# Kernel tuning notes

Measured on AMD Instinct MI355X. Metric: run time of the kernel, lower is better.

Reference implementation:

```python
import jax, jax.numpy as jnp
import numpy as np

N_NODES = 100000
N_EDGES = 1600000
IN_DIM = 128
OUT_DIM = 128
ALPHA = 0.2  # leaky relu negative slope
EPS = 9e-15


def setup_inputs() -> dict:
    key = jax.random.key(0)
    k1, k2, k3, k4, k5 = jax.random.split(key, 5)
    x = jax.random.normal(k1, (N_NODES, IN_DIM), dtype=jnp.float32)
    src = jax.random.randint(k2, (N_EDGES,), 0, N_NODES)
    dst = jax.random.randint(k3, (N_EDGES,), 0, N_NODES)
    edge_index = jnp.stack([src, dst]).astype(jnp.int64)
    # xavier-normal-ish params
    W = jax.random.normal(k4, (IN_DIM, OUT_DIM), dtype=jnp.float32) * (1.414 * np.sqrt(2.0 / (IN_DIM + OUT_DIM)))
    attn = jax.random.normal(k5, (1, 2 * OUT_DIM), dtype=jnp.float32) * (1.414 * np.sqrt(2.0 / (1 + 2 * OUT_DIM)))
    return {"x": x, "edge_index": edge_index, "W": W, "attn": attn}


def reference(x, edge_index, W, attn):
    N = x.shape[0]
    h = x @ W  # [N, out_dim]
    d = h.shape[1]
    a_src, a_dst = attn[0, :d], attn[0, d:]
    src, dst = edge_index[0], edge_index[1]
    # attn @ cat(h[src], h[dst]) == (h @ a_src)[src] + (h @ a_dst)[dst]
    values = (h @ a_src)[src] + (h @ a_dst)[dst]  # [E]
    e_a = jnp.where(values > 0, values, ALPHA * values)  # leaky relu
    edge_e = jnp.exp(e_a - jnp.max(e_a))  # [E]
    rowsum = jax.ops.segment_sum(edge_e, src, num_segments=N)  # [N]
    h_prime = jax.ops.segment_sum(edge_e[:, None] * h[dst], src, num_segments=N)  # [N, d]
    h_prime = h_prime / (rowsum[:, None] + EPS)
    return jax.nn.elu(h_prime)
```

## Files before the change

kernel.cpp:

```cpp
#include <hip/hip_runtime.h>
#include <hip/hip_bf16.h>
#include <stdint.h>


#define NN 100000
#define NE 1600000
#define DIM 128
#define ALPHA_ 0.2f
#define EPS_ 9e-15f

#define NSB 391
#define SBCAP 4608
#define CHUNK 4096
#define SDEG 56

typedef short bf16x8 __attribute__((ext_vector_type(8)));
typedef float floatx4 __attribute__((ext_vector_type(4)));

static __device__ __forceinline__ float bflo(unsigned u){ return __uint_as_float(u << 16); }
static __device__ __forceinline__ float bfhi(unsigned u){ return __uint_as_float(u & 0xFFFF0000u); }
static __device__ __forceinline__ float bfs(unsigned short s){ return __uint_as_float((unsigned)s << 16); }
static __device__ __forceinline__ unsigned short f2bf(float f){
  unsigned b = __float_as_uint(f);
  unsigned r = (b + 0x7FFFu + ((b >> 16) & 1u)) >> 16;
  return (unsigned short)r;
}
static __device__ __forceinline__ unsigned short f2bf_rhu(float f){
  return (unsigned short)((__float_as_uint(f) + 0x8000u) >> 16);
}
static __device__ __forceinline__ unsigned fkey(float f){
  unsigned u = __float_as_uint(f);
  return (u & 0x80000000u) ? ~u : (u | 0x80000000u);
}
static __device__ __forceinline__ float dkey(unsigned k){
  unsigned u = (k & 0x80000000u) ? (k ^ 0x80000000u) : ~k;
  return __uint_as_float(u);
}

__global__ __launch_bounds__(256) void k_detect(const unsigned short* W, const unsigned* EI,
                                                const unsigned short* attn, int* flags,
                                                unsigned short* attnb){
  __shared__ int sh_f, sh_e;
  int tid = threadIdx.x;
  if (tid == 0){ sh_f = 0; sh_e = 0; }
  __syncthreads();
  for (int i = tid; i < 1024; i += 256){
    unsigned u = W[i];
    unsigned e = (u >> 7) & 0xFF;
    if (e >= 0x85) sh_f = 1;
  }
  int any = 0;
  for (int k = tid; k < 2048; k += 256) any |= EI[2 * k + 1];
  atomicOr(&sh_e, any);
  __syncthreads();
  if (tid == 0){ flags[0] = sh_f; flags[1] = (sh_e == 0) ? 1 : 0; }
  __syncthreads();
  attnb[tid] = sh_f ? f2bf(((const float*)attn)[tid]) : attn[tid];
}

__global__ __launch_bounds__(256) void k_setup(const void* W, const int* flags,
                                               int* sbcnt, unsigned* keys, unsigned short* Wt){
  int i = blockIdx.x * 256 + threadIdx.x;
  if (i < NSB) sbcnt[i] = 0;
  if (i < 2) keys[i] = 0u;
  if (i < DIM * DIM){
    int k = i >> 7, n = i & 127;
    unsigned short v = flags[0] ? f2bf(((const float*)W)[i]) : ((const unsigned short*)W)[i];
    Wt[n * DIM + k] = v;
  }
}

__global__ __launch_bounds__(256, 4) void k_gemm(const void* X, const int* flags,
                                                 const unsigned short* Wt,
                                                 const unsigned short* attnb,
                                                 unsigned short* H, float* s1, float* s2,
                                                 unsigned* keys){
  __shared__ char wlds[32768];
  __shared__ float sm1[4], sm2[4];
  int tid = threadIdx.x;
  int wid = tid >> 6, lane = tid & 63;
  int m = lane & 15, q = lane >> 4;
  int rb = blockIdx.x * 64 + wid * 16;
  int row = rb + m;
  bool rok = row < NN;
  int fx32 = flags[0];

  for (int j = tid; j < 2048; j += 256){
    int wr = j >> 4, ch = j & 15;
    uint4 v = ((const uint4*)Wt)[j];
    *(uint4*)(wlds + ((wr * 16 + (ch ^ (wr & 15))) << 4)) = v;
  }
  __syncthreads();

  floatx4 acc[8];
  #pragma unroll
  for (int t = 0; t < 8; t++){ acc[t][0]=0.f; acc[t][1]=0.f; acc[t][2]=0.f; acc[t][3]=0.f; }
  #pragma unroll
  for (int ki = 0; ki < 4; ki++){
    int k0 = ki * 32 + q * 8;
    bf16x8 a;
    #pragma unroll
    for (int j = 0; j < 8; j++) a[j] = 0;
    if (rok){
      if (fx32){
        const float* xr = (const float*)X + (size_t)row * DIM + k0;
        float4 f0 = ((const float4*)xr)[0];
        float4 f1 = ((const float4*)xr)[1];
        a[0] = (short)f2bf_rhu(f0.x); a[1] = (short)f2bf_rhu(f0.y);
        a[2] = (short)f2bf_rhu(f0.z); a[3] = (short)f2bf_rhu(f0.w);
        a[4] = (short)f2bf_rhu(f1.x); a[5] = (short)f2bf_rhu(f1.y);
        a[6] = (short)f2bf_rhu(f1.z); a[7] = (short)f2bf_rhu(f1.w);
      } else {
        a = *(const bf16x8*)((const unsigned short*)X + (size_t)row * DIM + k0);
      }
    }
    #pragma unroll
    for (int t = 0; t < 8; t++){
      int rowb = t * 16 + m;
      bf16x8 b = *(const bf16x8*)(wlds + ((rowb * 16 + ((ki * 4 + q) ^ m)) << 4));
      acc[t] = __builtin_amdgcn_mfma_f32_16x16x32_bf16(a, b, acc[t], 0, 0, 0);
    }
  }

  float as[8], ad[8];
  #pragma unroll
  for (int t = 0; t < 8; t++){
    as[t] = bfs(attnb[t * 16 + m]);
    ad[t] = bfs(attnb[DIM + t * 16 + m]);
  }
  float lm1 = -3.0e38f, lm2 = -3.0e38f;
  #pragma unroll
  for (int r = 0; r < 4; r++){
    int grow = rb + q * 4 + r;
    float p1 = 0.f, p2 = 0.f;
    #pragma unroll
    for (int t = 0; t < 8; t++){ p1 += acc[t][r] * as[t]; p2 += acc[t][r] * ad[t]; }
    #pragma unroll
    for (int off = 1; off < 16; off <<= 1){
      p1 += __shfl_xor(p1, off);
      p2 += __shfl_xor(p2, off);
    }
    if (grow < NN){
      if (m == 0){ s1[grow] = p1; s2[grow] = p2; }
      lm1 = fmaxf(lm1, p1); lm2 = fmaxf(lm2, p2);
    }
  }
  #pragma unroll
  for (int off = 32; off; off >>= 1){
    lm1 = fmaxf(lm1, __shfl_xor(lm1, off));
    lm2 = fmaxf(lm2, __shfl_xor(lm2, off));
  }
  if (lane == 0){ sm1[wid] = lm1; sm2[wid] = lm2; }
  __syncthreads();
  if (tid == 0){
    float fa = fmaxf(fmaxf(sm1[0], sm1[1]), fmaxf(sm1[2], sm1[3]));
    float fb = fmaxf(fmaxf(sm2[0], sm2[1]), fmaxf(sm2[2], sm2[3]));
    atomicMax(&keys[0], fkey(fa));
    atomicMax(&keys[1], fkey(fb));
  }

  char* wb = wlds + wid * 8192;
  #pragma unroll
  for (int r = 0; r < 4; r++){
    int trow = q * 4 + r;
    #pragma unroll
    for (int t = 0; t < 8; t++){
      int col = t * 16 + m;
      int boff = trow * 256 + (((((col >> 3) ^ trow) & 15)) << 4) + ((col & 7) << 1);
      *(unsigned short*)(wb + boff) = f2bf(acc[t][r]);
    }
  }
  __syncthreads();
  int lrow = lane >> 2;
  int grow2 = rb + lrow;
  #pragma unroll
  for (int u = 0; u < 4; u++){
    int c = u * 4 + (lane & 3);
    uint4 v = *(const uint4*)(wb + lrow * 256 + (((c ^ lrow) & 15) << 4));
    if (grow2 < NN) *(uint4*)(H + (size_t)grow2 * DIM + c * 8) = v;
  }
}

static __device__ __forceinline__ void load_edge(const int* EI, int e64, int e,
                                                 int& s, int& d){
  if (e64){
    const long long* E64 = (const long long*)EI;
    s = (int)E64[e];
    d = (int)E64[NE + e];
  } else {
    s = EI[e];
    d = EI[NE + e];
  }
}

__global__ __launch_bounds__(256) void k_part(const int* EI, const int* flags,
                                              int* sbcnt, unsigned* sbbins){
  __shared__ unsigned sout[CHUNK];
  __shared__ unsigned short sg16[CHUNK];
  __shared__ int hist[NSB + 1];
  __shared__ int cur[NSB];
  __shared__ int base[NSB];
  int tid = threadIdx.x;
  int e0 = blockIdx.x * CHUNK;
  int nmy = NE - e0; if (nmy > CHUNK) nmy = CHUNK;
  int e64 = flags[1];

  for (int i = tid; i < NSB; i += 256) hist[i] = 0;
  __syncthreads();

  unsigned ent[16]; int sbv[16];
  #pragma unroll
  for (int i = 0; i < 16; i++){
    int idx = tid + i * 256;
    if (idx < nmy){
      int s, d;
      load_edge(EI, e64, e0 + idx, s, d);
      ent[i] = ((unsigned)(s & 255) << 17) | (unsigned)d;
      sbv[i] = s >> 8;
      atomicAdd(&hist[sbv[i]], 1);
    } else {
      ent[i] = 0u; sbv[i] = -1;
    }
  }
  __syncthreads();

  if (tid < 64){
    int carry = 0;
    #pragma unroll
    for (int rr = 0; rr < (NSB + 64) / 64; rr++){
      int idx = rr * 64 + tid;
      int v = (idx < NSB) ? hist[idx] : 0;
      int x = v;
      #pragma unroll
      for (int off = 1; off < 64; off <<= 1){
        int y = __shfl_up(x, off);
        if (tid >= off) x += y;
      }
      if (idx < NSB) hist[idx] = x - v + carry;
      carry += __shfl(x, 63);
    }
    if (tid == 0) hist[NSB] = carry;
  }
  __syncthreads();

  for (int t = tid; t < NSB; t += 256){
    cur[t] = 0;
    int h = hist[t + 1] - hist[t];
    base[t] = h ? atomicAdd(&sbcnt[t], h) : 0;
  }
  __syncthreads();

  #pragma unroll
  for (int i = 0; i < 16; i++){
    if (sbv[i] >= 0){
      int sb = sbv[i];
      int r = atomicAdd(&cur[sb], 1);
      int p = hist[sb] + r;
      int g = base[sb] + r;
      sout[p] = ent[i];
      sg16[p] = (g < SBCAP) ? (unsigned short)g : (unsigned short)0xFFFF;
    }
  }
  __syncthreads();

  for (int p = tid; p < nmy; p += 256){
    int lo = 0, hi = NSB;
    while (hi - lo > 1){
      int mid = (lo + hi) >> 1;
      if (hist[mid] <= p) lo = mid; else hi = mid;
    }
    unsigned short g = sg16[p];
    if (g != (unsigned short)0xFFFF)
      sbbins[(size_t)lo * SBCAP + g] = sout[p];
  }
}

__global__ __launch_bounds__(256) void k_sbagg(const int* sbcnt, const unsigned* sbbins,
                                               const float* s1, const float* s2,
                                               const unsigned* keys,
                                               const unsigned short* H, float* out){
  __shared__ int lcnt[64];
  __shared__ int llist[64][SDEG];
  int b = blockIdx.x >> 2;
  int qt = blockIdx.x & 3;
  int tid = threadIdx.x;
  if (tid < 64) lcnt[tid] = 0;
  __syncthreads();
  int n = sbcnt[b]; if (n > SBCAP) n = SBCAP;
  const unsigned* bp = sbbins + (size_t)b * SBCAP;
  int n4 = n & ~3;
  for (int i = tid * 4; i < n4; i += 1024){
    uint4 e4 = *(const uint4*)(bp + i);
    #pragma unroll
    for (int u = 0; u < 4; u++){
      unsigned ent = (&e4.x)[u];
      int sl = ent >> 17;
      if ((sl >> 6) == qt){
        int l = sl & 63;
        int p = atomicAdd(&lcnt[l], 1);
        if (p < SDEG) llist[l][p] = ent & 0x1FFFF;
      }
    }
  }
  for (int i = n4 + tid; i < n; i += 256){
    unsigned ent = bp[i];
    int sl = ent >> 17;
    if ((sl >> 6) == qt){
      int l = sl & 63;
      int p = atomicAdd(&lcnt[l], 1);
      if (p < SDEG) llist[l][p] = ent & 0x1FFFF;
    }
  }
  __syncthreads();
  float V = dkey(keys[0]) + dkey(keys[1]);
  float M = V > 0.f ? V : ALPHA_ * V;
  int wid = tid >> 6, lane = tid & 63;
  const unsigned* h2 = (const unsigned*)H;
  for (int sl = wid; sl < 64; sl += 4){
    int srcn = b * 256 + qt * 64 + sl;
    if (srcn >= NN) break;
    int deg = lcnt[sl]; if (deg > SDEG) deg = SDEG;
    float s1n = s1[srcn];
    int pd = 0; float pw = 0.f;
    if (lane < deg){
      pd = llist[sl][lane];
      float v = s1n + s2[pd];
      float va = v > 0.f ? v : ALPHA_ * v;
      pw = __expf(va - M);
    }
    float a0 = 0.f, a1 = 0.f, wsum = 0.f;
    int j = 0;
    for (; j + 4 <= deg; j += 4){
      int d0 = __shfl(pd, j), d1 = __shfl(pd, j + 1), d2 = __shfl(pd, j + 2), d3 = __shfl(pd, j + 3);
      float w0 = __shfl(pw, j), w1 = __shfl(pw, j + 1), w2 = __shfl(pw, j + 2), w3 = __shfl(pw, j + 3);
      unsigned v0 = h2[d0 * 64 + lane];
      unsigned v1 = h2[d1 * 64 + lane];
      unsigned v2 = h2[d2 * 64 + lane];
      unsigned v3 = h2[d3 * 64 + lane];
      a0 += w0 * bflo(v0) + w1 * bflo(v1) + w2 * bflo(v2) + w3 * bflo(v3);
      a1 += w0 * bfhi(v0) + w1 * bfhi(v1) + w2 * bfhi(v2) + w3 * bfhi(v3);
      wsum += (w0 + w1) + (w2 + w3);
    }
    for (; j < deg; j++){
      int d = __shfl(pd, j); float w = __shfl(pw, j);
      unsigned v = h2[d * 64 + lane];
      a0 += w * bflo(v); a1 += w * bfhi(v); wsum += w;
    }
    float r = wsum + EPS_;
    float p0 = a0 / r, p1 = a1 / r;
    float o0 = p0 > 0.f ? p0 : expm1f(p0);
    float o1 = p1 > 0.f ? p1 : expm1f(p1);
    ((float2*)out)[srcn * 64 + lane] = make_float2(o0, o1);
  }
}

extern "C" void kernel_launch(void* const* d_in, const int* in_sizes, int n_in,
                              void* d_out, int out_size, void* d_ws, size_t ws_size,
                              hipStream_t stream){
  (void)in_sizes; (void)n_in; (void)out_size; (void)ws_size;
  const void* X    = d_in[0];
  const int*  EI   = (const int*)d_in[1];
  const void* W    = d_in[2];
  const void* attn = d_in[3];

  char* ws = (char*)d_ws;
  size_t off = 0;
  auto alloc = [&](size_t bytes) -> char* {
    char* p = ws + off;
    off += (bytes + 255) & ~(size_t)255;
    return p;
  };
  unsigned short* H      = (unsigned short*)alloc((size_t)NN * DIM * 2);
  unsigned*       sbbins = (unsigned*)alloc((size_t)NSB * SBCAP * 4);
  unsigned short* Wt     = (unsigned short*)alloc(DIM * DIM * 2);
  unsigned short* attnb  = (unsigned short*)alloc(256 * 2);
  int*            flags  = (int*)alloc(2 * 4);
  float*          s1     = (float*)alloc(NN * 4);
  float*          s2     = (float*)alloc(NN * 4);
  int*            sbcnt  = (int*)alloc(NSB * 4);
  unsigned*       keys   = (unsigned*)alloc(2 * 4);
  float*          outp   = (float*)d_out;

  k_detect<<<1, 256, 0, stream>>>((const unsigned short*)W, (const unsigned*)EI,
                                  (const unsigned short*)attn, flags, attnb);
  k_setup<<<(NN + 255) / 256, 256, 0, stream>>>(W, flags, sbcnt, keys, Wt);
  k_gemm<<<(NN + 63) / 64, 256, 0, stream>>>(X, flags, Wt, attnb, H, s1, s2, keys);
  k_part<<<(NE + CHUNK - 1) / CHUNK, 256, 0, stream>>>(EI, flags, sbcnt, sbbins);
  k_sbagg<<<NSB * 4, 256, 0, stream>>>(sbcnt, sbbins, s1, s2, keys, H, outp);
}
```

Before: 251.7 us.

## Merge detect/setup kernels and fuse GEMM with edge partition in one launch

Combines the flag-detection and weight-transpose setup into one 66-block init kernel, where each block recomputes the fp32 flag locally so it no longer has to wait on a separate launch. The GEMM and the edge-partition kernels are fused into a single launch that interleaves four GEMM blocks with one partition block, sharing one static LDS buffer. The aim is to cut launch count and the tail gaps between kernels, and to overlap the compute-bound GEMM with the memory-bound partitioning. In exchange, the fused kernel reserves the larger LDS footprint for every block and runs under the GEMM's launch bounds, which may reduce occupancy for the partition blocks.

```diff
diff --git a/kernel.cpp b/kernel.cpp
--- a/kernel.cpp
+++ b/kernel.cpp
@@ -37,50 +37,69 @@
   return __uint_as_float(u);
 }
 
-__global__ __launch_bounds__(256) void k_detect(const unsigned short* W, const unsigned* EI,
-                                                const unsigned short* attn, int* flags,
-                                                unsigned short* attnb){
+__global__ __launch_bounds__(256) void k_init(const unsigned short* W, const unsigned* EI,
+                                              const unsigned short* attn, int* flags,
+                                              unsigned short* attnb, int* sbcnt,
+                                              unsigned* keys, unsigned short* Wt){
   __shared__ int sh_f, sh_e;
-  int tid = threadIdx.x;
-  if (tid == 0){ sh_f = 0; sh_e = 0; }
-  __syncthreads();
-  for (int i = tid; i < 1024; i += 256){
-    unsigned u = W[i];
-    unsigned e = (u >> 7) & 0xFF;
-    if (e >= 0x85) sh_f = 1;
-  }
-  int any = 0;
-  for (int k = tid; k < 2048; k += 256) any |= EI[2 * k + 1];
-  atomicOr(&sh_e, any);
-  __syncthreads();
-  if (tid == 0){ flags[0] = sh_f; flags[1] = (sh_e == 0) ? 1 : 0; }
-  __syncthreads();
-  attnb[tid] = sh_f ? f2bf(((const float*)attn)[tid]) : attn[tid];
-}
-
-__global__ __launch_bounds__(256) void k_setup(const void* W, const int* flags,
-                                               int* sbcnt, unsigned* keys, unsigned short* Wt){
-  int i = blockIdx.x * 256 + threadIdx.x;
-  if (i < NSB) sbcnt[i] = 0;
-  if (i < 2) keys[i] = 0u;
-  if (i < DIM * DIM){
+  int b = blockIdx.x, tid = threadIdx.x;
+  if (b == 0){
+    if (tid == 0){ sh_f = 0; sh_e = 0; }
+    __syncthreads();
+    for (int i = tid; i < 1024; i += 256){
+      unsigned u = W[i];
+      if (((u >> 7) & 0xFF) >= 0x85) sh_f = 1;
+    }
+    int any = 0;
+    for (int k = tid; k < 2048; k += 256) any |= EI[2 * k + 1];
+    atomicOr(&sh_e, any);
+    __syncthreads();
+    if (tid == 0){ flags[0] = sh_f; flags[1] = (sh_e == 0) ? 1 : 0; }
+    __syncthreads();
+    attnb[tid] = sh_f ? f2bf(((const float*)attn)[tid]) : attn[tid];
+  } else if (b == 65){
+    for (int i = tid; i < NSB; i += 256) sbcnt[i] = 0;
+    if (tid < 2) keys[tid] = 0u;
+  } else {
+    if (tid == 0) sh_f = 0;
+    __syncthreads();
+    for (int i = tid; i < 1024; i += 256){
+      unsigned u = W[i];
+      if (((u >> 7) & 0xFF) >= 0x85) sh_f = 1;
+    }
+    __syncthreads();
+    int i = (b - 1) * 256 + tid;
     int k = i >> 7, n = i & 127;
-    unsigned short v = flags[0] ? f2bf(((const float*)W)[i]) : ((const unsigned short*)W)[i];
+    unsigned short v = sh_f ? f2bf(((const float*)W)[i]) : ((const unsigned short*)W)[i];
     Wt[n * DIM + k] = v;
   }
 }
 
-__global__ __launch_bounds__(256, 4) void k_gemm(const void* X, const int* flags,
+static __device__ __forceinline__ void load_edge(const int* EI, int e64, int e,
+                                                 int& s, int& d){
+  if (e64){
+    const long long* E64 = (const long long*)EI;
+    s = (int)E64[e];
+    d = (int)E64[NE + e];
+  } else {
+    s = EI[e];
+    d = EI[NE + e];
+  }
+}
+
+static __device__ __forceinline__ void gemm_path(int gid, char* smem,
+                                                 const void* X, const int* flags,
                                                  const unsigned short* Wt,
                                                  const unsigned short* attnb,
                                                  unsigned short* H, float* s1, float* s2,
                                                  unsigned* keys){
-  __shared__ char wlds[32768];
-  __shared__ float sm1[4], sm2[4];
+  char* wlds = smem;
+  float* sm1 = (float*)(smem + 32768);
+  float* sm2 = sm1 + 4;
   int tid = threadIdx.x;
   int wid = tid >> 6, lane = tid & 63;
   int m = lane & 15, q = lane >> 4;
-  int rb = blockIdx.x * 64 + wid * 16;
+  int rb = gid * 64 + wid * 16;
   int row = rb + m;
   bool rok = row < NN;
   int fx32 = flags[0];
@@ -117,8 +136,8 @@
     #pragma unroll
     for (int t = 0; t < 8; t++){
       int rowb = t * 16 + m;
-      bf16x8 b = *(const bf16x8*)(wlds + ((rowb * 16 + ((ki * 4 + q) ^ m)) << 4));
-      acc[t] = __builtin_amdgcn_mfma_f32_16x16x32_bf16(a, b, acc[t], 0, 0, 0);
+      bf16x8 bfr = *(const bf16x8*)(wlds + ((rowb * 16 + ((ki * 4 + q) ^ m)) << 4));
+      acc[t] = __builtin_amdgcn_mfma_f32_16x16x32_bf16(a, bfr, acc[t], 0, 0, 0);
     }
   }
 
@@ -181,27 +200,16 @@
   }
 }
 
-static __device__ __forceinline__ void load_edge(const int* EI, int e64, int e,
-                                                 int& s, int& d){
-  if (e64){
-    const long long* E64 = (const long long*)EI;
-    s = (int)E64[e];
-    d = (int)E64[NE + e];
-  } else {
-    s = EI[e];
-    d = EI[NE + e];
-  }
-}
-
-__global__ __launch_bounds__(256) void k_part(const int* EI, const int* flags,
-                                              int* sbcnt, unsigned* sbbins){
-  __shared__ unsigned sout[CHUNK];
-  __shared__ unsigned short sg16[CHUNK];
-  __shared__ int hist[NSB + 1];
-  __shared__ int cur[NSB];
-  __shared__ int base[NSB];
+static __device__ __forceinline__ void part_path(int pid, char* smem,
+                                                 const int* EI, const int* flags,
+                                                 int* sbcnt, unsigned* sbbins){
+  unsigned* sout = (unsigned*)smem;
+  unsigned short* sg16 = (unsigned short*)(smem + 16384);
+  int* hist = (int*)(smem + 24576);
+  int* cur  = (int*)(smem + 26144);
+  int* base = (int*)(smem + 27708);
   int tid = threadIdx.x;
-  int e0 = blockIdx.x * CHUNK;
+  int e0 = pid * CHUNK;
   int nmy = NE - e0; if (nmy > CHUNK) nmy = CHUNK;
   int e64 = flags[1];
 
@@ -272,6 +280,23 @@
     unsigned short g = sg16[p];
     if (g != (unsigned short)0xFFFF)
       sbbins[(size_t)lo * SBCAP + g] = sout[p];
+  }
+}
+
+__global__ __launch_bounds__(256, 4) void k_main(const void* X, const int* EI,
+                                                 const int* flags,
+                                                 const unsigned short* Wt,
+                                                 const unsigned short* attnb,
+                                                 unsigned short* H, float* s1, float* s2,
+                                                 unsigned* keys, int* sbcnt,
+                                                 unsigned* sbbins){
+  __shared__ char smem[32800];
+  int bid = blockIdx.x;
+  int T = bid / 5, r = bid % 5;
+  if (r == 4){
+    part_path(T, smem, EI, flags, sbcnt, sbbins);
+  } else {
+    gemm_path(T * 4 + r, smem, X, flags, Wt, attnb, H, s1, s2, keys);
   }
 }
 
@@ -381,10 +406,10 @@
   unsigned*       keys   = (unsigned*)alloc(2 * 4);
   float*          outp   = (float*)d_out;
 
-  k_detect<<<1, 256, 0, stream>>>((const unsigned short*)W, (const unsigned*)EI,
-                                  (const unsigned short*)attn, flags, attnb);
-  k_setup<<<(NN + 255) / 256, 256, 0, stream>>>(W, flags, sbcnt, keys, Wt);
-  k_gemm<<<(NN + 63) / 64, 256, 0, stream>>>(X, flags, Wt, attnb, H, s1, s2, keys);
-  k_part<<<(NE + CHUNK - 1) / CHUNK, 256, 0, stream>>>(EI, flags, sbcnt, sbbins);
+  k_init<<<66, 256, 0, stream>>>((const unsigned short*)W, (const unsigned*)EI,
+                                 (const unsigned short*)attn, flags, attnb,
+                                 sbcnt, keys, Wt);
+  k_main<<<NSB * 5, 256, 0, stream>>>(X, EI, flags, Wt, attnb, H, s1, s2,
+                                      keys, sbcnt, sbbins);
   k_sbagg<<<NSB * 4, 256, 0, stream>>>(sbcnt, sbbins, s1, s2, keys, H, outp);
 }
```

Result: faster. 235.3 us (-6.5%).
